# Kernel optimization log

Hardware: AMD Instinct MI355X
Metric: run time of the kernel (lower is better)

The kernel has to match this reference:

```python
import jax, jax.numpy as jnp
import numpy as np
from functools import partial

B, L, TAPS, NMODES = 64, 4096, 32, 2
LR_W = 1.0 / 2**6   # assumed fixed LMS step for w (MetaNone: updates = -lr * grad)
LR_F = 1.0 / 2**7   # assumed fixed LMS step for f
GRAD_MAX = 30.0     # grad_max[0]
EPS = 1e-9


def setup_inputs() -> dict:
    key = jax.random.key(0)
    ks = jax.random.split(key, 6)
    u_r = jax.random.normal(ks[0], (B, L, TAPS, NMODES), jnp.float32)
    u_i = jax.random.normal(ks[1], (B, L, TAPS, NMODES), jnp.float32)
    x_r = jax.random.normal(ks[2], (B, L, NMODES), jnp.float32)
    x_i = jax.random.normal(ks[3], (B, L, NMODES), jnp.float32)
    # gauss_init: gaussian window, normalized, tiled to [B, Nmodes, Nmodes, taps]
    y = jnp.exp(-jnp.linspace(-5.0, 5.0, TAPS) ** 2)
    y = y / jnp.sum(y)
    w0_r = jnp.broadcast_to(y, (B, NMODES, NMODES, TAPS)).astype(jnp.float32)
    w0_i = jnp.zeros((B, NMODES, NMODES, TAPS), jnp.float32)
    f0_r = jnp.ones((B, NMODES), jnp.float32)
    f0_i = jnp.zeros((B, NMODES), jnp.float32)
    return dict(u_r=u_r, u_i=u_i, x_r=x_r, x_i=x_i,
                w0_r=w0_r, w0_i=w0_i, f0_r=f0_r, f0_i=f0_i)


def _adf_step(carry, inp):
    w, f = carry                      # w: [B,Nm,Nm,T] c64, f: [B,Nm] c64
    u_t, x_t = inp                    # u_t: [B,T,Nm], x_t: [B,Nm]
    v = jnp.einsum('bijt,btj->bi', w, u_t)          # mimo output [B,Nm]
    k = v * f
    d = x_t                                          # train mode: truth symbol
    psi_hat = jnp.abs(f) / f
    e_w = d * psi_hat - v
    e_f = d - k
    # normalized gradients (ddlms => normalized_grad=True)
    u_energy = jnp.sum(jnp.abs(u_t) ** 2, axis=(1, 2)) + EPS   # [B]
    uc = jnp.conjugate(jnp.swapaxes(u_t, 1, 2))                # [B,Nm,T]
    gw = -(1.0 / u_energy)[:, None, None, None] * e_w[:, :, None, None] * uc[:, None, :, :]
    v_energy = jnp.sum(jnp.abs(v) ** 2, axis=1) + EPS          # [B]
    gf = -(1.0 / v_energy)[:, None] * e_f * jnp.conjugate(v)
    ag = jnp.abs(gf)
    safe = jnp.where(ag > GRAD_MAX, ag, 1.0)
    gf = jnp.where(ag > GRAD_MAX, gf / safe * GRAD_MAX, gf)
    # MetaNone/LMS update: theta += -lr * grad
    w = w - LR_W * gw
    f = f - LR_F * gf
    return (w, f), k


def reference(u_r, u_i, x_r, x_i, w0_r, w0_i, f0_r, f0_i):
    u = u_r + 1j * u_i                # [B,L,T,Nm] complex64
    x = x_r + 1j * x_i                # [B,L,Nm]
    w0 = w0_r + 1j * w0_i
    f0 = f0_r + 1j * f0_i
    u_seq = jnp.swapaxes(u, 0, 1)     # [L,B,T,Nm] time-major for scan
    x_seq = jnp.swapaxes(x, 0, 1)     # [L,B,Nm]
    (_, _), z = jax.lax.scan(_adf_step, (w0, f0), (u_seq, x_seq))
    z = jnp.swapaxes(z, 0, 1)         # [B,L,Nm] equalized symbols
    return jnp.stack([z.real, z.imag], axis=-1)  # [B,L,Nm,2] float view
```

## Files before the change

kernel.cpp:

```cpp
#include <hip/hip_runtime.h>

namespace {

constexpr int kB = 64;
constexpr int kL = 4096;
constexpr float kLrW = 1.0f / 64.0f;
constexpr float kLrF = 1.0f / 128.0f;
constexpr float kGradMax = 30.0f;
constexpr float kEps = 1e-9f;
constexpr int kPF = 8;
constexpr int kNC = kL / kPF;

#define DPP_ADD_F32(v, ctrl)                                                   \
    v += __int_as_float(__builtin_amdgcn_update_dpp(                           \
        0, __float_as_int(v), (ctrl), 0xF, 0xF, true))

__device__ __forceinline__ float rl(float v, int l) {
    return __int_as_float(__builtin_amdgcn_readlane(__float_as_int(v), l));
}
__device__ __forceinline__ float frcp(float x) { return __builtin_amdgcn_rcpf(x); }
__device__ __forceinline__ float frsq(float x) { return __builtin_amdgcn_rsqf(x); }

__device__ __forceinline__ void cfma(float2& a, const float2 s, const float2 u) {
    asm("v_pk_fma_f32 %0, %1, %2, %0 op_sel:[1,1,0] op_sel_hi:[1,0,1] neg_lo:[0,1,0]\n\t"
        "v_pk_fma_f32 %0, %1, %2, %0 op_sel:[0,0,0] op_sel_hi:[0,1,1]"
        : "+v"(a) : "v"(s), "v"(u));
}
__device__ __forceinline__ void cfma_conj(float2& a, const float2 s, const float2 u) {
    asm("v_pk_fma_f32 %0, %1, %2, %0 op_sel:[1,1,0] op_sel_hi:[1,0,1]\n\t"
        "v_pk_fma_f32 %0, %1, %2, %0 op_sel:[0,0,0] op_sel_hi:[0,1,1] neg_hi:[0,1,0]"
        : "+v"(a) : "v"(s), "v"(u));
}
__device__ __forceinline__ float2 cmul(const float2 s, const float2 u) {
    float2 r;
    asm("v_pk_mul_f32 %0, %1, %2 op_sel:[1,1] op_sel_hi:[1,0] neg_lo:[0,1]\n\t"
        "v_pk_fma_f32 %0, %1, %2, %0 op_sel:[0,0,0] op_sel_hi:[0,1,1]"
        : "=&v"(r) : "v"(s), "v"(u));
    return r;
}
__device__ __forceinline__ float2 cmul_conj(const float2 s, const float2 u) {
    float2 r;
    asm("v_pk_mul_f32 %0, %1, %2 op_sel:[1,1] op_sel_hi:[1,0]\n\t"
        "v_pk_fma_f32 %0, %1, %2, %0 op_sel:[0,0,0] op_sel_hi:[0,1,1] neg_hi:[0,1,0]"
        : "=&v"(r) : "v"(s), "v"(u));
    return r;
}
__device__ __forceinline__ float2 pk_fnma(const float2 s, const float2 u, const float2 c) {
    float2 r;
    asm("v_pk_fma_f32 %0, %1, %2, %3 neg_lo:[1,0,0] neg_hi:[1,0,0]"
        : "=v"(r) : "v"(s), "v"(u), "v"(c));
    return r;
}
__device__ __forceinline__ float2 pk_sub(const float2 a, const float2 b) {
    float2 r;
    asm("v_pk_add_f32 %0, %1, %2 neg_lo:[0,1] neg_hi:[0,1]" : "=v"(r) : "v"(a), "v"(b));
    return r;
}
__device__ __forceinline__ float2 pk_mul(const float2 a, const float2 b) {
    float2 r;
    asm("v_pk_mul_f32 %0, %1, %2" : "=v"(r) : "v"(a), "v"(b));
    return r;
}

typedef unsigned u32x2v __attribute__((ext_vector_type(2)));
__device__ __forceinline__ float pairsum16(float v) {
    u32x2v r = __builtin_amdgcn_permlane16_swap(__float_as_uint(v),
                                                __float_as_uint(v), false, false);
    return __uint_as_float(r[0]) + __uint_as_float(r[1]);
}
__device__ __forceinline__ float pairsum32(float v) {
    u32x2v r = __builtin_amdgcn_permlane32_swap(__float_as_uint(v),
                                                __float_as_uint(v), false, false);
    return __uint_as_float(r[0]) + __uint_as_float(r[1]);
}
__device__ __forceinline__ float rowsum16(float v) {
    DPP_ADD_F32(v, 0x121); DPP_ADD_F32(v, 0x122);
    DPP_ADD_F32(v, 0x124); DPP_ADD_F32(v, 0x128);
    return v;
}

__global__ __launch_bounds__(256, 1) void pre_kernel(
    const float* __restrict__ u_r, const float* __restrict__ u_i,
    const float* __restrict__ x_r, const float* __restrict__ x_i,
    float* __restrict__ meta)
{
    const int lane = threadIdx.x & 63;
    const int idx = blockIdx.x * 4 + (threadIdx.x >> 6);
    const float a = u_r[(size_t)idx * 64 + lane];
    const float c = u_i[(size_t)idx * 64 + lane];
    float e = fmaf(a, a, c * c);
    e = rowsum16(e);
    e = pairsum16(e);
    e = pairsum32(e);
    if (lane == 0) {
        const float su = kLrW * frcp(e + kEps);
        const float2 xr = *(const float2*)(x_r + (size_t)idx * 2);
        const float2 xi = *(const float2*)(x_i + (size_t)idx * 2);
        float4* m = (float4*)(meta + (size_t)idx * 8);
        m[0] = make_float4(su, su, xr.x, xi.x);
        m[1] = make_float4(xr.y, xi.y, 0.0f, 0.0f);
    }
}

__global__ __launch_bounds__(64, 1) void adf_kernel(
    const float* __restrict__ u_r, const float* __restrict__ u_i,
    const float* __restrict__ w0r_g, const float* __restrict__ w0i_g,
    const float* __restrict__ f0r_g, const float* __restrict__ f0i_g,
    const float* __restrict__ meta, float* __restrict__ out)
{
    const int b = blockIdx.x;
    const int lane = threadIdx.x;
    const int half = lane >> 5;
    const int tap  = lane & 31;

    const int wbase = b * 128 + half * 64 + tap;
    float2 wA = make_float2(w0r_g[wbase],      w0i_g[wbase]);
    float2 wB = make_float2(w0r_g[wbase + 32], w0i_g[wbase + 32]);

    float2 f2 = make_float2(f0r_g[b * 2 + half], f0i_g[b * 2 + half]);
    float invf = frsq(fmaf(f2.x, f2.x, f2.y * f2.y));

    const float2* __restrict__ ur2 = (const float2*)u_r + (size_t)b * kL * 32;
    const float2* __restrict__ ui2 = (const float2*)u_i + (size_t)b * kL * 32;
    const float* __restrict__ mp = meta + (size_t)b * kL * 8;
    float2* __restrict__ ob2 = (float2*)out + (size_t)b * kL * 2;

    float2 Au[kPF], Aq[kPF], Asu[kPF], Ad[kPF];
    float2 Bu[kPF], Bq[kPF], Bsu[kPF], Bd[kPF];
    float2 kO[kPF];
    float2 sdp2 = make_float2(0.f, 0.f);

    auto loadChunk = [&](float2 (&u)[kPF], float2 (&q)[kPF],
                         float2 (&su)[kPF], float2 (&d)[kPF], int chunk) {
#pragma unroll
        for (int s = 0; s < kPF; ++s) {
            int t = chunk * kPF + s;
            t = t < kL ? t : kL - 1;
            u[s]  = ur2[(size_t)t * 32 + tap];
            q[s]  = ui2[(size_t)t * 32 + tap];
            su[s] = *(const float2*)(mp + (size_t)t * 8);
            d[s]  = *(const float2*)(mp + (size_t)t * 8 + 2 + 2 * half);
        }
        __builtin_amdgcn_sched_barrier(0);
    };

    auto mk_sdp = [&](const float2 su, const float2 d) {
        const float2 P = cmul_conj(d, f2);
        const float g = su.x * invf;
        return pk_mul(make_float2(g, g), P);
    };

    auto body = [&](int s, float2 (&u)[kPF], float2 (&q)[kPF],
                    float2 (&su)[kPF], float2 (&d)[kPF], bool first) {
        const float2 cA = make_float2(u[s].x, q[s].x);
        const float2 cB = make_float2(u[s].y, q[s].y);
        if (first) {
            sdp2 = mk_sdp(su[0], d[0]);
        }
        float2 p = cmul(wA, cA);
        cfma(p, wB, cB);
        float pr = p.x, pi = p.y;
        DPP_ADD_F32(pr, 0x111); DPP_ADD_F32(pi, 0x111);
        DPP_ADD_F32(pr, 0x112); DPP_ADD_F32(pi, 0x112);
        DPP_ADD_F32(pr, 0x114); DPP_ADD_F32(pi, 0x114);
        DPP_ADD_F32(pr, 0x118); DPP_ADD_F32(pi, 0x118);
        DPP_ADD_F32(pr, 0x142); DPP_ADD_F32(pi, 0x142);
        const float v0r = rl(pr, 31), v1r = rl(pr, 63);
        const float v0i = rl(pi, 31), v1i = rl(pi, 63);
        const float2 v2 = make_float2(half ? v1r : v0r, half ? v1i : v0i);

        const float2 tau = pk_fnma(su[s], v2, sdp2);
        cfma_conj(wA, tau, cA);
        cfma_conj(wB, tau, cB);

        const float2 k2 = cmul(v2, f2);
        kO[s] = k2;
        const float2 ef = pk_sub(d[s], k2);
        float ven = v0r * v0r;
        ven = fmaf(v0i, v0i, ven);
        ven = fmaf(v1r, v1r, ven);
        ven = fmaf(v1i, v1i, ven);
        const float nv = frcp(ven + kEps);
        const float2 H = cmul_conj(ef, v2);
        const float MH = fmaf(H.x, H.x, H.y * H.y);
        const float sc = fminf(nv, kGradMax * frsq(MH));
        const float scl = kLrF * sc;
        f2.x = fmaf(scl, H.x, f2.x);
        f2.y = fmaf(scl, H.y, f2.y);
        invf = frsq(fmaf(f2.x, f2.x, f2.y * f2.y));
        if (s + 1 < kPF) {
            sdp2 = mk_sdp(su[s + 1], d[s + 1]);
        }
    };

    auto processChunk = [&](int tbase, float2 (&u)[kPF], float2 (&q)[kPF],
                            float2 (&su)[kPF], float2 (&d)[kPF]) {
#pragma unroll
        for (int s = 0; s < kPF; ++s)
            body(s, u, q, su, d, s == 0);
        if (tap == 0) {
#pragma unroll
            for (int s = 0; s < kPF; ++s)
                ob2[(size_t)(tbase + s) * 2 + half] = kO[s];
        }
    };

    loadChunk(Au, Aq, Asu, Ad, 0);
    loadChunk(Bu, Bq, Bsu, Bd, 1);

    for (int c = 0; c < kNC; c += 2) {
        processChunk(c * kPF, Au, Aq, Asu, Ad);
        loadChunk(Au, Aq, Asu, Ad, (c + 2 < kNC) ? c + 2 : kNC - 1);
        processChunk((c + 1) * kPF, Bu, Bq, Bsu, Bd);
        loadChunk(Bu, Bq, Bsu, Bd, (c + 3 < kNC) ? c + 3 : kNC - 1);
    }
}

__global__ __launch_bounds__(64, 1) void adf_fb(
    const float* __restrict__ u_r, const float* __restrict__ u_i,
    const float* __restrict__ x_r, const float* __restrict__ x_i,
    const float* __restrict__ w0r_g, const float* __restrict__ w0i_g,
    const float* __restrict__ f0r_g, const float* __restrict__ f0i_g,
    float* __restrict__ out)
{
    const int b = blockIdx.x;
    const int lane = threadIdx.x;
    const int half = lane >> 5;
    const int tap  = lane & 31;
    const bool lo  = (half == 0);

    const int wbase = b * 128 + half * 64 + tap;
    float wAr = w0r_g[wbase],      wAi = w0i_g[wbase];
    float wBr = w0r_g[wbase + 32], wBi = w0i_g[wbase + 32];

    float fr = f0r_g[b * 2 + half];
    float fi = f0i_g[b * 2 + half];
    const float invf0 = frsq(fmaf(fr, fr, fi * fi));
    float psr = fr * invf0, psm = -fi * invf0;

    const float2* __restrict__ ur2 = (const float2*)u_r + (size_t)b * kL * 32;
    const float2* __restrict__ ui2 = (const float2*)u_i + (size_t)b * kL * 32;
    const float2* __restrict__ xr2 = (const float2*)x_r + (size_t)b * kL;
    const float2* __restrict__ xi2 = (const float2*)x_i + (size_t)b * kL;
    float2* __restrict__ ob2 = (float2*)out + (size_t)b * kL * 2;

    float2 Au[kPF], Aq[kPF], AxR[kPF], AxI[kPF];
    float2 Bu[kPF], Bq[kPF], BxR[kPF], BxI[kPF];
    float suA[kPF], suB[kPF];
    float kR[kPF], kI[kPF];
    float sdpr = 0.0f, sdpi = 0.0f;

    auto loadChunk = [&](float2 (&u)[kPF], float2 (&q)[kPF],
                         float2 (&xR)[kPF], float2 (&xI)[kPF], int chunk) {
#pragma unroll
        for (int s = 0; s < kPF; ++s) {
            int t = chunk * kPF + s;
            t = t < kL ? t : kL - 1;
            u[s]  = ur2[(size_t)t * 32 + tap];
            q[s]  = ui2[(size_t)t * 32 + tap];
            xR[s] = xr2[t];
            xI[s] = xi2[t];
        }
        __builtin_amdgcn_sched_barrier(0);
    };

    auto calcSu = [&](float2 (&u)[kPF], float2 (&q)[kPF], float (&su)[kPF]) {
        float e[kPF];
#pragma unroll
        for (int s = 0; s < kPF; ++s) {
            float t0 = u[s].x * u[s].x;
            t0 = fmaf(u[s].y, u[s].y, t0);
            t0 = fmaf(q[s].x, q[s].x, t0);
            t0 = fmaf(q[s].y, q[s].y, t0);
            e[s] = t0;
        }
#pragma unroll
        for (int s = 0; s < kPF; ++s) { DPP_ADD_F32(e[s], 0x111); }
#pragma unroll
        for (int s = 0; s < kPF; ++s) { DPP_ADD_F32(e[s], 0x112); }
#pragma unroll
        for (int s = 0; s < kPF; ++s) { DPP_ADD_F32(e[s], 0x114); }
#pragma unroll
        for (int s = 0; s < kPF; ++s) { DPP_ADD_F32(e[s], 0x118); }
#pragma unroll
        for (int s = 0; s < kPF; ++s) { DPP_ADD_F32(e[s], 0x142); }
#pragma unroll
        for (int s = 0; s < kPF; ++s) su[s] = kLrW * frcp(rl(e[s], 31) + kEps);
    };

    auto body = [&](int s, float2 (&u)[kPF], float2 (&q)[kPF],
                    float2 (&xR)[kPF], float2 (&xI)[kPF], float (&su)[kPF],
                    bool first) {
        const float2 uc = u[s], qc = q[s];
        if (first) {
            const float dr0 = lo ? xR[0].x : xR[0].y;
            const float di0 = lo ? xI[0].x : xI[0].y;
            sdpr = su[0] * fmaf(dr0, psr, -di0 * psm);
            sdpi = su[0] * fmaf(dr0, psm,  di0 * psr);
        }
        float pr = wAr * uc.x;
        pr = fmaf(-wAi, qc.x, pr); pr = fmaf(wBr, uc.y, pr); pr = fmaf(-wBi, qc.y, pr);
        float pi = wAr * qc.x;
        pi = fmaf(wAi, uc.x, pi); pi = fmaf(wBr, qc.y, pi); pi = fmaf(wBi, uc.y, pi);
        DPP_ADD_F32(pr, 0x111); DPP_ADD_F32(pi, 0x111);
        DPP_ADD_F32(pr, 0x112); DPP_ADD_F32(pi, 0x112);
        DPP_ADD_F32(pr, 0x114); DPP_ADD_F32(pi, 0x114);
        DPP_ADD_F32(pr, 0x118); DPP_ADD_F32(pi, 0x118);
        DPP_ADD_F32(pr, 0x142); DPP_ADD_F32(pi, 0x142);
        const float v0r = rl(pr, 31), v1r = rl(pr, 63);
        const float v0i = rl(pi, 31), v1i = rl(pi, 63);
        const float vr = lo ? v0r : v1r;
        const float vi = lo ? v0i : v1i;

        const float sun = su[s];
        const float tr = fmaf(-sun, vr, sdpr);
        const float ti = fmaf(-sun, vi, sdpi);
        wAr = fmaf(tr, uc.x, fmaf(ti, qc.x, wAr));
        wAi = fmaf(ti, uc.x, fmaf(-tr, qc.x, wAi));
        wBr = fmaf(tr, uc.y, fmaf(ti, qc.y, wBr));
        wBi = fmaf(ti, uc.y, fmaf(-tr, qc.y, wBi));

        const float dr = lo ? xR[s].x : xR[s].y;
        const float di = lo ? xI[s].x : xI[s].y;
        const float kr = fmaf(vr, fr, -vi * fi);
        const float ki = fmaf(vr, fi,  vi * fr);
        kR[s] = kr; kI[s] = ki;
        const float efr = dr - kr, efi = di - ki;
        float ven = v0r * v0r;
        ven = fmaf(v0i, v0i, ven);
        ven = fmaf(v1r, v1r, ven);
        ven = fmaf(v1i, v1i, ven);
        const float nv = frcp(ven + kEps);
        float hr = efr * vr; hr = fmaf(efi, vi, hr);
        float hi = efi * vr; hi = fmaf(-efr, vi, hi);
        hr *= nv; hi *= nv;
        float mg = hr * hr; mg = fmaf(hi, hi, mg);
        const float sc = fminf(1.0f, kGradMax * frsq(mg));
        const float scl = kLrF * sc;
        fr = fmaf(scl, hr, fr);
        fi = fmaf(scl, hi, fi);
        const float invf = frsq(fmaf(fr, fr, fi * fi));
        psr = fr * invf; psm = -fi * invf;
        if (s + 1 < kPF) {
            const float dnr = lo ? xR[s + 1].x : xR[s + 1].y;
            const float dni = lo ? xI[s + 1].x : xI[s + 1].y;
            sdpr = su[s + 1] * fmaf(dnr, psr, -dni * psm);
            sdpi = su[s + 1] * fmaf(dnr, psm,  dni * psr);
        }
    };

    auto processChunk = [&](int tbase, float2 (&u)[kPF], float2 (&q)[kPF],
                            float2 (&xR)[kPF], float2 (&xI)[kPF], float (&su)[kPF]) {
#pragma unroll
        for (int s = 0; s < kPF; ++s)
            body(s, u, q, xR, xI, su, s == 0);
        if (tap == 0) {
#pragma unroll
            for (int s = 0; s < kPF; ++s)
                ob2[(size_t)(tbase + s) * 2 + half] = make_float2(kR[s], kI[s]);
        }
    };

    loadChunk(Au, Aq, AxR, AxI, 0);
    loadChunk(Bu, Bq, BxR, BxI, 1);
    calcSu(Au, Aq, suA);

    for (int c = 0; c < kNC; c += 2) {
        processChunk(c * kPF, Au, Aq, AxR, AxI, suA);
        loadChunk(Au, Aq, AxR, AxI, (c + 2 < kNC) ? c + 2 : kNC - 1);
        calcSu(Bu, Bq, suB);
        processChunk((c + 1) * kPF, Bu, Bq, BxR, BxI, suB);
        loadChunk(Bu, Bq, BxR, BxI, (c + 3 < kNC) ? c + 3 : kNC - 1);
        calcSu(Au, Aq, suA);
    }
}

}

extern "C" void kernel_launch(void* const* d_in, const int* in_sizes, int n_in,
                              void* d_out, int out_size, void* d_ws, size_t ws_size,
                              hipStream_t stream) {
    const float* u_r  = (const float*)d_in[0];
    const float* u_i  = (const float*)d_in[1];
    const float* x_r  = (const float*)d_in[2];
    const float* x_i  = (const float*)d_in[3];
    const float* w0_r = (const float*)d_in[4];
    const float* w0_i = (const float*)d_in[5];
    const float* f0_r = (const float*)d_in[6];
    const float* f0_i = (const float*)d_in[7];
    float* out = (float*)d_out;

    const size_t need = (size_t)kB * kL * 8 * sizeof(float);
    if (ws_size >= need) {
        float* meta = (float*)d_ws;
        pre_kernel<<<dim3(kB * kL / 4), dim3(256), 0, stream>>>(u_r, u_i, x_r, x_i, meta);
        adf_kernel<<<dim3(kB), dim3(64), 0, stream>>>(
            u_r, u_i, w0_r, w0_i, f0_r, f0_i, meta, out);
    } else {
        adf_fb<<<dim3(kB), dim3(64), 0, stream>>>(
            u_r, u_i, x_r, x_i, w0_r, w0_i, f0_r, f0_i, out);
    }
}
```

Before: 720.1 us.

## Software-pipeline the next step's dot-product reduction with the current f update

Restructures the per-step loop so the w update for step t is applied first. The next step's dot product and DPP lane reduction are then issued and interleaved with step t's scalar filter update (k, error, gradient clipping, f and invf). A prologue primes the first reduction, and each chunk receives the first sample of the following chunk so the pipeline crosses chunk boundaries. The aim is to hide DPP and readlane latency on the serial recurrence critical path, at the cost of more live registers and more complex control flow.

```diff
diff --git a/kernel.cpp b/kernel.cpp
--- a/kernel.cpp
+++ b/kernel.cpp
@@ -129,6 +129,7 @@
     float2 Bu[kPF], Bq[kPF], Bsu[kPF], Bd[kPF];
     float2 kO[kPF];
     float2 sdp2 = make_float2(0.f, 0.f);
+    float prC = 0.f, piC = 0.f;
 
     auto loadChunk = [&](float2 (&u)[kPF], float2 (&q)[kPF],
                          float2 (&su)[kPF], float2 (&d)[kPF], int chunk) {
@@ -150,13 +151,78 @@
         return pk_mul(make_float2(g, g), P);
     };
 
-    auto body = [&](int s, float2 (&u)[kPF], float2 (&q)[kPF],
-                    float2 (&su)[kPF], float2 (&d)[kPF], bool first) {
-        const float2 cA = make_float2(u[s].x, q[s].x);
-        const float2 cB = make_float2(u[s].y, q[s].y);
-        if (first) {
-            sdp2 = mk_sdp(su[0], d[0]);
-        }
+    auto body = [&](int s, const float2 cA, const float2 cB,
+                    const float2 nA, const float2 nB,
+                    const float2 suc, const float2 dc,
+                    const float2 sun, const float2 dn) {
+        const float v0r = rl(prC, 31), v1r = rl(prC, 63);
+        const float v0i = rl(piC, 31), v1i = rl(piC, 63);
+        const float2 v2 = make_float2(half ? v1r : v0r, half ? v1i : v0i);
+
+        const float2 tau = pk_fnma(suc, v2, sdp2);
+        cfma_conj(wA, tau, cA);
+        cfma_conj(wB, tau, cB);
+
+        float2 p = cmul(wA, nA);
+        cfma(p, wB, nB);
+        float pr = p.x, pi = p.y;
+
+        DPP_ADD_F32(pr, 0x111); DPP_ADD_F32(pi, 0x111);
+        const float2 k2 = cmul(v2, f2);
+        kO[s] = k2;
+        DPP_ADD_F32(pr, 0x112); DPP_ADD_F32(pi, 0x112);
+        const float2 ef = pk_sub(dc, k2);
+        DPP_ADD_F32(pr, 0x114); DPP_ADD_F32(pi, 0x114);
+        float ven = v0r * v0r;
+        ven = fmaf(v0i, v0i, ven);
+        ven = fmaf(v1r, v1r, ven);
+        ven = fmaf(v1i, v1i, ven);
+        DPP_ADD_F32(pr, 0x118); DPP_ADD_F32(pi, 0x118);
+        const float nv = frcp(ven + kEps);
+        const float2 H = cmul_conj(ef, v2);
+        DPP_ADD_F32(pr, 0x142); DPP_ADD_F32(pi, 0x142);
+        prC = pr; piC = pi;
+
+        const float MH = fmaf(H.x, H.x, H.y * H.y);
+        const float sc = fminf(nv, kGradMax * frsq(MH));
+        const float scl = kLrF * sc;
+        f2.x = fmaf(scl, H.x, f2.x);
+        f2.y = fmaf(scl, H.y, f2.y);
+        invf = frsq(fmaf(f2.x, f2.x, f2.y * f2.y));
+        sdp2 = mk_sdp(sun, dn);
+    };
+
+    auto processChunk = [&](int tbase, float2 (&u)[kPF], float2 (&q)[kPF],
+                            float2 (&su)[kPF], float2 (&d)[kPF],
+                            const float2 nu0, const float2 nq0,
+                            const float2 su0n, const float2 d0n) {
+#pragma unroll
+        for (int s = 0; s < kPF; ++s) {
+            const float2 cA = make_float2(u[s].x, q[s].x);
+            const float2 cB = make_float2(u[s].y, q[s].y);
+            float2 nA, nB, sun, dn;
+            if (s + 1 < kPF) {
+                nA = make_float2(u[s + 1].x, q[s + 1].x);
+                nB = make_float2(u[s + 1].y, q[s + 1].y);
+                sun = su[s + 1]; dn = d[s + 1];
+            } else {
+                nA = nu0; nB = nq0; sun = su0n; dn = d0n;
+            }
+            body(s, cA, cB, nA, nB, su[s], d[s], sun, dn);
+        }
+        if (tap == 0) {
+#pragma unroll
+            for (int s = 0; s < kPF; ++s)
+                ob2[(size_t)(tbase + s) * 2 + half] = kO[s];
+        }
+    };
+
+    loadChunk(Au, Aq, Asu, Ad, 0);
+    loadChunk(Bu, Bq, Bsu, Bd, 1);
+
+    {
+        const float2 cA = make_float2(Au[0].x, Aq[0].x);
+        const float2 cB = make_float2(Au[0].y, Aq[0].y);
         float2 p = cmul(wA, cA);
         cfma(p, wB, cB);
         float pr = p.x, pi = p.y;
@@ -165,53 +231,18 @@
         DPP_ADD_F32(pr, 0x114); DPP_ADD_F32(pi, 0x114);
         DPP_ADD_F32(pr, 0x118); DPP_ADD_F32(pi, 0x118);
         DPP_ADD_F32(pr, 0x142); DPP_ADD_F32(pi, 0x142);
-        const float v0r = rl(pr, 31), v1r = rl(pr, 63);
-        const float v0i = rl(pi, 31), v1i = rl(pi, 63);
-        const float2 v2 = make_float2(half ? v1r : v0r, half ? v1i : v0i);
-
-        const float2 tau = pk_fnma(su[s], v2, sdp2);
-        cfma_conj(wA, tau, cA);
-        cfma_conj(wB, tau, cB);
-
-        const float2 k2 = cmul(v2, f2);
-        kO[s] = k2;
-        const float2 ef = pk_sub(d[s], k2);
-        float ven = v0r * v0r;
-        ven = fmaf(v0i, v0i, ven);
-        ven = fmaf(v1r, v1r, ven);
-        ven = fmaf(v1i, v1i, ven);
-        const float nv = frcp(ven + kEps);
-        const float2 H = cmul_conj(ef, v2);
-        const float MH = fmaf(H.x, H.x, H.y * H.y);
-        const float sc = fminf(nv, kGradMax * frsq(MH));
-        const float scl = kLrF * sc;
-        f2.x = fmaf(scl, H.x, f2.x);
-        f2.y = fmaf(scl, H.y, f2.y);
-        invf = frsq(fmaf(f2.x, f2.x, f2.y * f2.y));
-        if (s + 1 < kPF) {
-            sdp2 = mk_sdp(su[s + 1], d[s + 1]);
-        }
-    };
-
-    auto processChunk = [&](int tbase, float2 (&u)[kPF], float2 (&q)[kPF],
-                            float2 (&su)[kPF], float2 (&d)[kPF]) {
-#pragma unroll
-        for (int s = 0; s < kPF; ++s)
-            body(s, u, q, su, d, s == 0);
-        if (tap == 0) {
-#pragma unroll
-            for (int s = 0; s < kPF; ++s)
-                ob2[(size_t)(tbase + s) * 2 + half] = kO[s];
-        }
-    };
-
-    loadChunk(Au, Aq, Asu, Ad, 0);
-    loadChunk(Bu, Bq, Bsu, Bd, 1);
+        prC = pr; piC = pi;
+        sdp2 = mk_sdp(Asu[0], Ad[0]);
+    }
 
     for (int c = 0; c < kNC; c += 2) {
-        processChunk(c * kPF, Au, Aq, Asu, Ad);
+        processChunk(c * kPF, Au, Aq, Asu, Ad,
+                     make_float2(Bu[0].x, Bq[0].x), make_float2(Bu[0].y, Bq[0].y),
+                     Bsu[0], Bd[0]);
         loadChunk(Au, Aq, Asu, Ad, (c + 2 < kNC) ? c + 2 : kNC - 1);
-        processChunk((c + 1) * kPF, Bu, Bq, Bsu, Bd);
+        processChunk((c + 1) * kPF, Bu, Bq, Bsu, Bd,
+                     make_float2(Au[0].x, Aq[0].x), make_float2(Au[0].y, Aq[0].y),
+                     Asu[0], Ad[0]);
         loadChunk(Bu, Bq, Bsu, Bd, (c + 3 < kNC) ? c + 3 : kNC - 1);
     }
 }
```

After: 704.4 us, median of 2. 2.2% less time.
